# Optimization experiments

Hardware: AMD Instinct MI355X
Metric: run time of the kernel (lower is better)

Reference implementation:

```python
import jax, jax.numpy as jnp
import numpy as np
import math

B, S, D, H = 2, 2048, 2048, 16
DH = D // H
NEG = -1e9  # finite stand-in for -inf so fully-masked rows stay NaN-free


def setup_inputs() -> dict:
    key = jax.random.key(0)
    ks = jax.random.split(key, 6)
    x = jax.random.normal(ks[0], (B, S, D), dtype=jnp.float32)
    key_padding_mask = jax.random.randint(ks[1], (B, S), 0, 2, dtype=jnp.int32)
    Wqkv_w = jax.random.normal(ks[2], (3 * D, D), dtype=jnp.float32) / math.sqrt(D)
    Wqkv_b = jnp.zeros((3 * D,), dtype=jnp.float32)
    out_w = jax.random.normal(ks[3], (D, D), dtype=jnp.float32) / math.sqrt(D)
    out_b = jnp.zeros((D,), dtype=jnp.float32)
    return {"x": x, "key_padding_mask": key_padding_mask, "Wqkv_w": Wqkv_w,
            "Wqkv_b": Wqkv_b, "out_w": out_w, "out_b": out_b}


def reference(x, key_padding_mask, Wqkv_w, Wqkv_b, out_w, out_b):
    b, s, d = x.shape
    # fused QKV projection (torch Linear: y = x @ W.T + b)
    qkv = (x @ Wqkv_w.T + Wqkv_b).reshape(b, s, 3, H, DH)
    q, k, v = qkv[:, :, 0], qkv[:, :, 1], qkv[:, :, 2]  # each [b, s, H, DH]
    scale = 1.0 / math.sqrt(DH)
    scores = jnp.einsum('bqhd,bkhd->bhqk', q, k) * scale  # [b, H, s, s]
    # additive key-padding bias: -inf where mask == 0 (finite NEG for stability)
    pad_bias = jnp.where(key_padding_mask == 0, NEG, 0.0).astype(x.dtype)[:, None, None, :]
    # causal mask: key index > query index is disallowed
    causal = jnp.where(jnp.arange(s)[None, :] > jnp.arange(s)[:, None], NEG, 0.0).astype(x.dtype)
    p = jax.nn.softmax(scores + pad_bias + causal, axis=-1)
    attn = jnp.einsum('bhqk,bkhd->bqhd', p, v).reshape(b, s, d)
    return attn @ out_w.T + out_b
```

## Files before the change

kernel.cpp:

```cpp
#include <hip/hip_runtime.h>
#include <cstdint>

typedef unsigned short u16;
typedef __attribute__((ext_vector_type(8))) short short8v;
typedef __attribute__((ext_vector_type(8))) unsigned short u16x8;
typedef __attribute__((ext_vector_type(4))) float floatx4;

typedef unsigned int __attribute__((address_space(1))) as1_u32;
typedef unsigned int __attribute__((address_space(3))) as3_u32;

__device__ __forceinline__ u16 f2bf(float f) {
  union { float f; unsigned u; } v; v.f = f;
  unsigned r = v.u + 0x7FFFu + ((v.u >> 16) & 1u);
  return (u16)(r >> 16);
}

__device__ __forceinline__ unsigned cvt_pk_bf16(float lo, float hi) {
  unsigned r;
  asm("v_cvt_pk_bf16_f32 %0, %1, %2" : "=v"(r) : "v"(lo), "v"(hi));
  return r;
}

__device__ __forceinline__ void gload16(void* lds, const void* g) {
  __builtin_amdgcn_global_load_lds((as1_u32*)(uintptr_t)g, (as3_u32*)(uintptr_t)lds, 16, 0, 0);
}

__global__ __launch_bounds__(256)
void f2bf3_kernel(const float* __restrict__ in0, u16* __restrict__ out0, int n0,
                  const float* __restrict__ in1, u16* __restrict__ out1, int n1,
                  const float* __restrict__ in2, u16* __restrict__ out2, int n2) {
  int i = blockIdx.x * 256 + threadIdx.x;
  const int stride = gridDim.x * 256;
  const int total = n0 + n1 + n2;
  for (; i < total; i += stride) {
    const float* src; u16* dst; int k;
    if (i < n0)            { src = in0; dst = out0; k = i; }
    else if (i < n0 + n1)  { src = in1; dst = out1; k = i - n0; }
    else                   { src = in2; dst = out2; k = i - n0 - n1; }
    float4 v = ((const float4*)src)[k];
    ushort4 o;
    o.x = f2bf(v.x); o.y = f2bf(v.y); o.z = f2bf(v.z); o.w = f2bf(v.w);
    ((ushort4*)dst)[k] = o;
  }
}

__global__ __launch_bounds__(512, 4)
void gemm_qkv(const u16* __restrict__ A, const u16* __restrict__ B,
              const float* __restrict__ bias, u16* __restrict__ C,
              u16* __restrict__ VT, int M, int N, int K) {
  __shared__ u16 Al[3][4096];
  __shared__ u16 Bl[3][8192];
  const int tid = threadIdx.x;
  const int wid = tid >> 6, lane = tid & 63;
  const int wr = wid >> 2, wc = wid & 3;
  const int li = lane & 15, lg = lane >> 4;
  const int nwg = gridDim.x;
  const int bid = blockIdx.x;
  const int swz = (bid & 7) * (nwg >> 3) + (bid >> 3);
  const int mcnt = M >> 7;
  const int bm = swz % mcnt, bn = swz / mcnt;
  const int brow = bm * 128, bcol = bn * 256;
  const int NT = K >> 5;

  const int P = tid * 16;
  const int pr = P >> 7;
  const int innerLog = (P & 127) ^ ((pr & 7) << 4);
  const int srow = (pr << 1) + (innerLog >> 6);
  const int skb = innerLog & 63;
  const u16* aS = A + (size_t)(brow + srow) * K + (skb >> 1);
  const u16* bS = B + (size_t)(bcol + srow) * K + (skb >> 1);

#define STG(slot, kt_)                                                          \
  {                                                                             \
    const u16* a_ = aS + (kt_) * 32;                                            \
    const u16* b_ = bS + (kt_) * 32;                                            \
    gload16((char*)&Al[slot][0] + P, a_);                                       \
    gload16((char*)&Bl[slot][0] + P, b_);                                       \
    gload16((char*)&Bl[slot][0] + 8192 + P, b_ + (size_t)128 * K);              \
  }

  floatx4 acc[4][4];
#pragma unroll
  for (int m = 0; m < 4; ++m)
#pragma unroll
    for (int n = 0; n < 4; ++n) acc[m][n] = floatx4{0.f, 0.f, 0.f, 0.f};

  const int fxor = ((li >> 1) & 7) << 4;
  const int finner = (((li & 1) << 6) + (lg << 4)) ^ fxor;
  const int aoff = (wr * 32 + (li >> 1)) * 128 + finner;
  const int boff = (wc * 32 + (li >> 1)) * 128 + finner;

  STG(0, 0);
  STG(1, 1);
  asm volatile("s_waitcnt vmcnt(3)" ::: "memory");
  __builtin_amdgcn_s_barrier();

  int sl = 0;
  for (int t = 0; t < NT; ++t) {
    const char* Ab = (const char*)&Al[sl][0];
    const char* Bb = (const char*)&Bl[sl][0];
    short8v af[4], bf[4];
#pragma unroll
    for (int m = 0; m < 4; ++m) af[m] = *(const short8v*)(Ab + aoff + m * 1024);
#pragma unroll
    for (int n = 0; n < 4; ++n) bf[n] = *(const short8v*)(Bb + boff + n * 1024);

    int s2 = sl + 2; if (s2 >= 3) s2 -= 3;
    if (t + 2 < NT) STG(s2, t + 2);

    __builtin_amdgcn_s_setprio(1);
#pragma unroll
    for (int m = 0; m < 4; ++m)
#pragma unroll
      for (int n = 0; n < 4; ++n)
        acc[m][n] = __builtin_amdgcn_mfma_f32_16x16x32_bf16(af[m], bf[n], acc[m][n], 0, 0, 0);
    __builtin_amdgcn_s_setprio(0);

    if (t + 2 < NT)      asm volatile("s_waitcnt vmcnt(3)" ::: "memory");
    else if (t + 1 < NT) asm volatile("s_waitcnt vmcnt(0)" ::: "memory");
    __builtin_amdgcn_s_barrier();
    sl = (sl + 1 == 3) ? 0 : sl + 1;
  }
#undef STG

  const int crow0 = brow + wr * 64 + lg * 4;
  const int ccol0 = bcol + wc * 64 + li;
  if (bcol >= 4096) {
    const int bb = crow0 >> 11;
    const int s0b = (crow0 & 2047);
#pragma unroll
    for (int n = 0; n < 4; ++n) {
      const int vcol = ccol0 - 4096 + n * 16;
      const int hh = vcol >> 7, dh = vcol & 127;
      const float bv = bias[ccol0 + n * 16];
      u16* drow = VT + ((size_t)(bb * 16 + hh) * 128 + dh) * 2048;
#pragma unroll
      for (int m = 0; m < 4; ++m) {
        ushort4 o;
        o.x = f2bf(acc[m][n][0] + bv);
        o.y = f2bf(acc[m][n][1] + bv);
        o.z = f2bf(acc[m][n][2] + bv);
        o.w = f2bf(acc[m][n][3] + bv);
        *(ushort4*)(drow + s0b + m * 16) = o;
      }
    }
  } else {
#pragma unroll
    for (int n = 0; n < 4; ++n) {
      const float bv = bias[ccol0 + n * 16];
#pragma unroll
      for (int m = 0; m < 4; ++m) {
#pragma unroll
        for (int j = 0; j < 4; ++j) {
          const float v = acc[m][n][j] + bv;
          C[(size_t)(crow0 + m * 16 + j) * N + (ccol0 + n * 16)] = f2bf(v);
        }
      }
    }
  }
}

template <int OUT_BF16>
__global__ __launch_bounds__(256, 4)
void gemm_s(const u16* __restrict__ A, const u16* __restrict__ B,
            const float* __restrict__ bias, void* __restrict__ C,
            int M, int N, int K) {
  __shared__ u16 Al[3][4096];
  __shared__ u16 Bl[3][4096];
  const int tid = threadIdx.x;
  const int wid = tid >> 6, lane = tid & 63;
  const int wr = wid >> 1, wc = wid & 1;
  const int li = lane & 15, lg = lane >> 4;
  const int nwg = gridDim.x;
  const int bid = blockIdx.x;
  const int swz = (bid & 7) * (nwg >> 3) + (bid >> 3);
  const int mcnt = M >> 7;
  const int bm = swz % mcnt, bn = swz / mcnt;
  const int brow = bm * 128, bcol = bn * 128;
  const int NT = K >> 5;

  const int P = tid * 16;
  const int pr = P >> 7;
  const int innerLog = (P & 127) ^ ((pr & 7) << 4);
  const int srow = (pr << 1) + (innerLog >> 6);
  const int skb = innerLog & 63;
  const u16* aS = A + (size_t)(brow + srow) * K + (skb >> 1);
  const u16* bS = B + (size_t)(bcol + srow) * K + (skb >> 1);

#define STG(slot, kt_)                                                          \
  {                                                                             \
    const u16* a_ = aS + (kt_) * 32;                                            \
    const u16* b_ = bS + (kt_) * 32;                                            \
    gload16((char*)&Al[slot][0] + P, a_);                                       \
    gload16((char*)&Al[slot][0] + 4096 + P, a_ + (size_t)64 * K);               \
    gload16((char*)&Bl[slot][0] + P, b_);                                       \
    gload16((char*)&Bl[slot][0] + 4096 + P, b_ + (size_t)64 * K);               \
  }

  floatx4 acc[4][4];
#pragma unroll
  for (int m = 0; m < 4; ++m)
#pragma unroll
    for (int n = 0; n < 4; ++n) acc[m][n] = floatx4{0.f, 0.f, 0.f, 0.f};

  const int fxor = ((li >> 1) & 7) << 4;
  const int finner = (((li & 1) << 6) + (lg << 4)) ^ fxor;
  const int aoff = (wr * 32 + (li >> 1)) * 128 + finner;
  const int boff = (wc * 32 + (li >> 1)) * 128 + finner;

  STG(0, 0);
  STG(1, 1);
  asm volatile("s_waitcnt vmcnt(4)" ::: "memory");
  __builtin_amdgcn_s_barrier();

  int sl = 0;
  for (int t = 0; t < NT; ++t) {
    const char* Ab = (const char*)&Al[sl][0];
    const char* Bb = (const char*)&Bl[sl][0];
    short8v af[4], bf[4];
#pragma unroll
    for (int m = 0; m < 4; ++m) af[m] = *(const short8v*)(Ab + aoff + m * 1024);
#pragma unroll
    for (int n = 0; n < 4; ++n) bf[n] = *(const short8v*)(Bb + boff + n * 1024);

    int s2 = sl + 2; if (s2 >= 3) s2 -= 3;
    if (t + 2 < NT) STG(s2, t + 2);

    __builtin_amdgcn_s_setprio(1);
#pragma unroll
    for (int m = 0; m < 4; ++m)
#pragma unroll
      for (int n = 0; n < 4; ++n)
        acc[m][n] = __builtin_amdgcn_mfma_f32_16x16x32_bf16(af[m], bf[n], acc[m][n], 0, 0, 0);
    __builtin_amdgcn_s_setprio(0);

    if (t + 2 < NT)      asm volatile("s_waitcnt vmcnt(4)" ::: "memory");
    else if (t + 1 < NT) asm volatile("s_waitcnt vmcnt(0)" ::: "memory");
    __builtin_amdgcn_s_barrier();
    sl = (sl + 1 == 3) ? 0 : sl + 1;
  }
#undef STG

  const int crow0 = brow + wr * 64 + lg * 4;
  const int ccol0 = bcol + wc * 64 + li;
#pragma unroll
  for (int n = 0; n < 4; ++n) {
    const float bv = bias[ccol0 + n * 16];
#pragma unroll
    for (int m = 0; m < 4; ++m) {
#pragma unroll
      for (int j = 0; j < 4; ++j) {
        const float v = acc[m][n][j] + bv;
        const size_t idx = (size_t)(crow0 + m * 16 + j) * N + (ccol0 + n * 16);
        if (OUT_BF16) ((u16*)C)[idx] = f2bf(v);
        else          ((float*)C)[idx] = v;
      }
    }
  }
}

__global__ __launch_bounds__(256, 2)
void attn_fused(const u16* __restrict__ qkv, const u16* __restrict__ vt,
                const int* __restrict__ kpm, u16* __restrict__ attn_out) {
  constexpr int S = 2048, DQ = 6144;
  __shared__ u16 Kl[2][64 * 128];
  __shared__ u16 Vl[128 * 64];
  __shared__ float mskf[2048];
  __shared__ int s_any;
  const int bx = blockIdx.x, by = blockIdx.y;
  const int qt = ((by >> 4) & 1) ? bx : (15 - bx);
  const int bh = by;
  const int b = bh >> 4, h = bh & 15;
  const int tid = threadIdx.x, wave = tid >> 6, lane = tid & 63;
  const int lg = lane >> 4, li = lane & 15;
  const int qrow0 = qt * 128 + wave * 32;

  const u16* Qb = qkv + (size_t)b * S * DQ + h * 128;
  const u16* Kb = Qb + 2048;
  const u16* Vtb = vt + (size_t)bh * 128 * 2048;
  const int* mrow = kpm + b * S;

  if (tid == 0) s_any = 0;
  __syncthreads();
  {
    int a = 0;
    for (int j = tid; j < 2048; j += 256) {
      const int mv = mrow[j];
      mskf[j] = mv ? 0.f : -1.0e9f;
      if (mv && j <= qt * 128) a = 1;
    }
    if (a) s_any = 1;
  }
  __syncthreads();
  const int anyv = s_any;
  const int nt = anyv ? (2 * qt + 2) : 32;
  const int causalFromW = anyv ? (qrow0 >> 6) : 0;

  short8v qb[2][4];
#pragma unroll
  for (int m = 0; m < 2; ++m) {
    const u16* qp = Qb + (size_t)(qrow0 + m * 16 + li) * DQ + lg * 8;
#pragma unroll
    for (int kk = 0; kk < 4; ++kk) qb[m][kk] = *(const short8v*)(qp + kk * 32);
  }
  asm volatile("s_waitcnt vmcnt(0)" ::: "memory");

  float mM[2], lSum[2];
  floatx4 oa[2][8];
#pragma unroll
  for (int m = 0; m < 2; ++m) {
    mM[m] = -3.0e38f; lSum[m] = 0.f;
#pragma unroll
    for (int n = 0; n < 8; ++n) oa[m][n] = floatx4{0.f, 0.f, 0.f, 0.f};
  }

  const u16* kSrc[4]; const u16* vSrc[4];
#pragma unroll
  for (int i = 0; i < 4; ++i) {
    const int L = i * 4096 + tid * 16;
    const int r = L >> 8;
    const int c = ((L & 255) ^ ((r & 7) << 4)) >> 1;
    kSrc[i] = Kb + (size_t)r * DQ + c;
    const int d = L >> 7;
    const int sv = ((L & 127) ^ ((d & 7) << 4)) >> 1;
    vSrc[i] = Vtb + (size_t)d * 2048 + sv;
  }

#define STAGE_K(buf, kt_)                                                      \
  {                                                                            \
    const int kv0_ = (kt_) * 64;                                               \
    _Pragma("unroll")                                                          \
    for (int i = 0; i < 4; ++i)                                                \
      gload16((char*)Kl + (buf) * 16384 + i * 4096 + tid * 16,                 \
              kSrc[i] + (size_t)kv0_ * DQ);                                    \
  }
#define STAGE_V(kt_)                                                           \
  {                                                                            \
    const int kv0_ = (kt_) * 64;                                               \
    _Pragma("unroll")                                                          \
    for (int i = 0; i < 4; ++i)                                                \
      gload16((char*)Vl + i * 4096 + tid * 16, vSrc[i] + kv0_);                \
  }

  const float scale = 0.08838834764831845f;

  STAGE_K(0, 0);
  STAGE_V(0);

  for (int kt = 0; kt < nt; ++kt) {
    const int cur = kt & 1;
    const int kv0 = kt * 64;
    if (kt + 1 < nt) {
      STAGE_K(cur ^ 1, kt + 1);
      asm volatile("s_waitcnt vmcnt(8)" ::: "memory");
    } else {
      asm volatile("s_waitcnt vmcnt(4)" ::: "memory");
    }
    __builtin_amdgcn_s_barrier();

    const char* Kcur = (const char*)Kl + cur * 16384;

    floatx4 sc[2][4];
#pragma unroll
    for (int n = 0; n < 4; ++n) { sc[0][n] = floatx4{0,0,0,0}; sc[1][n] = floatx4{0,0,0,0}; }
    __builtin_amdgcn_s_setprio(1);
#pragma unroll
    for (int n = 0; n < 4; ++n) {
      const int r = n * 16 + li;
#pragma unroll
      for (int kk = 0; kk < 4; ++kk) {
        const int byteo = (r * 256 + kk * 64 + lg * 16) ^ ((r & 7) << 4);
        const short8v kf = *(const short8v*)(Kcur + byteo);
        sc[0][n] = __builtin_amdgcn_mfma_f32_16x16x32_bf16(kf, qb[0][kk], sc[0][n], 0, 0, 0);
        sc[1][n] = __builtin_amdgcn_mfma_f32_16x16x32_bf16(kf, qb[1][kk], sc[1][n], 0, 0, 0);
      }
    }
    __builtin_amdgcn_s_setprio(0);

    floatx4 pbv[4];
#pragma unroll
    for (int n = 0; n < 4; ++n)
      pbv[n] = *(const floatx4*)&mskf[kv0 + n * 16 + lg * 4];
    const bool cz = (kt >= causalFromW);

    short8v pf[2][2];
#pragma unroll
    for (int m = 0; m < 2; ++m) {
      const int q_l = qrow0 + m * 16 + li;
      float tmax = -3.0e38f;
#pragma unroll
      for (int n = 0; n < 4; ++n)
#pragma unroll
        for (int j = 0; j < 4; ++j) {
          float s = sc[m][n][j] * scale + pbv[n][j];
          if (cz && (kv0 + n * 16 + lg * 4 + j > q_l)) s -= 1.0e9f;
          sc[m][n][j] = s;
          tmax = fmaxf(tmax, s);
        }
      tmax = fmaxf(tmax, __shfl_xor(tmax, 16));
      tmax = fmaxf(tmax, __shfl_xor(tmax, 32));
      const float mnew = fmaxf(mM[m], tmax);
      const float f = __expf(mM[m] - mnew);
      mM[m] = mnew;
      float rs = 0.f;
#pragma unroll
      for (int n = 0; n < 4; ++n)
#pragma unroll
        for (int j = 0; j < 4; ++j) {
          const float e = __expf(sc[m][n][j] - mnew);
          sc[m][n][j] = e; rs += e;
        }
      rs += __shfl_xor(rs, 16);
      rs += __shfl_xor(rs, 32);
      lSum[m] = lSum[m] * f + rs;
#pragma unroll
      for (int n2 = 0; n2 < 8; ++n2) oa[m][n2] *= f;

      unsigned w32[4][2];
#pragma unroll
      for (int n = 0; n < 4; ++n) {
        w32[n][0] = cvt_pk_bf16(sc[m][n][0], sc[m][n][1]);
        w32[n][1] = cvt_pk_bf16(sc[m][n][2], sc[m][n][3]);
      }
      union PF { short8v s; unsigned w[4]; } pfu[2];
#pragma unroll
      for (int kk2 = 0; kk2 < 2; ++kk2) {
#pragma unroll
        for (int hh = 0; hh < 2; ++hh) {
          unsigned u = w32[2 * kk2][hh], v = w32[2 * kk2 + 1][hh];
          asm volatile("v_permlane32_swap_b32 %0, %1" : "+v"(u), "+v"(v));
          asm volatile("v_permlane16_swap_b32 %0, %1" : "+v"(u), "+v"(v));
          pfu[kk2].w[hh] = u;
          pfu[kk2].w[2 + hh] = v;
        }
      }
      pf[m][0] = pfu[0].s;
      pf[m][1] = pfu[1].s;
    }

    if (kt + 1 < nt) asm volatile("s_waitcnt vmcnt(4)" ::: "memory");
    else             asm volatile("s_waitcnt vmcnt(0)" ::: "memory");
    __builtin_amdgcn_s_barrier();

    __builtin_amdgcn_s_setprio(1);
#pragma unroll
    for (int kk2 = 0; kk2 < 2; ++kk2) {
#pragma unroll
      for (int n2 = 0; n2 < 8; ++n2) {
        const int d = n2 * 16 + li;
        const int vbyte = (d * 128 + kk2 * 64 + lg * 16) ^ ((d & 7) << 4);
        const short8v vf = *(const short8v*)((const char*)Vl + vbyte);
        oa[0][n2] = __builtin_amdgcn_mfma_f32_16x16x32_bf16(vf, pf[0][kk2], oa[0][n2], 0, 0, 0);
        oa[1][n2] = __builtin_amdgcn_mfma_f32_16x16x32_bf16(vf, pf[1][kk2], oa[1][n2], 0, 0, 0);
      }
    }
    __builtin_amdgcn_s_setprio(0);
    __builtin_amdgcn_s_barrier();
    if (kt + 1 < nt) STAGE_V(kt + 1);
  }

  {
    char* Ol = (char*)Kl + wave * 8192;
#pragma unroll
    for (int m = 0; m < 2; ++m) {
      const float inv = 1.0f / lSum[m];
      const int q_ = m * 16 + li;
#pragma unroll
      for (int n2 = 0; n2 < 8; ++n2) {
        unsigned lo = cvt_pk_bf16(oa[m][n2][0] * inv, oa[m][n2][1] * inv);
        unsigned hi = cvt_pk_bf16(oa[m][n2][2] * inv, oa[m][n2][3] * inv);
        const int byteo = (q_ * 256 + n2 * 32 + lg * 8) ^ ((q_ & 7) << 4);
        uint2 pr2; pr2.x = lo; pr2.y = hi;
        *(uint2*)(Ol + byteo) = pr2;
      }
    }
    asm volatile("s_waitcnt lgkmcnt(0)" ::: "memory");
#pragma unroll
    for (int rr = 0; rr < 4; ++rr) {
      const int r = rr * 8 + (lane >> 3);
      const size_t grow = (size_t)(b * 2048 + qt * 128 + wave * 32 + r) * 2048 + h * 128;
#pragma unroll
      for (int s2 = 0; s2 < 2; ++s2) {
        const int byteo = (r * 256 + (lane & 7) * 32 + s2 * 16) ^ ((r & 7) << 4);
        const u16x8 val = *(const u16x8*)(Ol + byteo);
        *(u16x8*)&attn_out[grow + (lane & 7) * 16 + s2 * 8] = val;
      }
    }
  }
#undef STAGE_K
#undef STAGE_V
}

extern "C" void kernel_launch(void* const* d_in, const int* in_sizes, int n_in,
                              void* d_out, int out_size, void* d_ws, size_t ws_size,
                              hipStream_t stream) {
  const float* x    = (const float*)d_in[0];
  const int*   kpm  = (const int*)d_in[1];
  const float* wqkv = (const float*)d_in[2];
  const float* bqkv = (const float*)d_in[3];
  const float* wout = (const float*)d_in[4];
  const float* bout = (const float*)d_in[5];
  float* out = (float*)d_out;

  char* ws = (char*)d_ws;
  u16* xbf   = (u16*)(ws);
  u16* wqbf  = (u16*)(ws + (16u << 20));
  u16* wobf  = (u16*)(ws + (40u << 20));
  u16* qkvb  = (u16*)(ws + (48u << 20));
  u16* vtb   = (u16*)(ws + (96u << 20));
  u16* attnb = (u16*)(ws + (112u << 20));

  f2bf3_kernel<<<2048, 256, 0, stream>>>(x,    xbf,  4096 * 2048 / 4,
                                         wqkv, wqbf, 6144 * 2048 / 4,
                                         wout, wobf, 2048 * 2048 / 4);

  gemm_qkv<<<768, 512, 0, stream>>>(xbf, wqbf, bqkv, qkvb, vtb, 4096, 6144, 2048);
  attn_fused<<<dim3(16, 32), 256, 0, stream>>>(qkvb, vtb, kpm, attnb);
  gemm_s<0><<<512, 256, 0, stream>>>(attnb, wobf, bout, out, 4096, 2048, 2048);
}
```

Measured before the change: 279.7 us.

## Double-buffer V tiles with K prefetch and use raw exp2 softmax

Adds a second V buffer in LDS so the next tile's K and V both load during the current iteration. This removes the mid-iteration wait and barrier before the PV matmul. It also folds log2(e) into the scale and mask constants so softmax can use the raw v_exp_f32 instruction instead of __expf. The cost is more LDS per block, which may reduce occupancy, and a full vmcnt(0) wait on the last tile.

```diff
diff --git a/kernel.cpp b/kernel.cpp
--- a/kernel.cpp
+++ b/kernel.cpp
@@ -18,6 +18,12 @@
 __device__ __forceinline__ unsigned cvt_pk_bf16(float lo, float hi) {
   unsigned r;
   asm("v_cvt_pk_bf16_f32 %0, %1, %2" : "=v"(r) : "v"(lo), "v"(hi));
+  return r;
+}
+
+__device__ __forceinline__ float exp2_raw(float x) {
+  float r;
+  asm("v_exp_f32 %0, %1" : "=v"(r) : "v"(x));
   return r;
 }
 
@@ -264,7 +270,7 @@
                 const int* __restrict__ kpm, u16* __restrict__ attn_out) {
   constexpr int S = 2048, DQ = 6144;
   __shared__ u16 Kl[2][64 * 128];
-  __shared__ u16 Vl[128 * 64];
+  __shared__ u16 Vl[2][64 * 128];
   __shared__ float mskf[2048];
   __shared__ int s_any;
   const int bx = blockIdx.x, by = blockIdx.y;
@@ -286,7 +292,7 @@
     int a = 0;
     for (int j = tid; j < 2048; j += 256) {
       const int mv = mrow[j];
-      mskf[j] = mv ? 0.f : -1.0e9f;
+      mskf[j] = mv ? 0.f : -1.4426950e9f;
       if (mv && j <= qt * 128) a = 1;
     }
     if (a) s_any = 1;
@@ -326,39 +332,36 @@
     vSrc[i] = Vtb + (size_t)d * 2048 + sv;
   }
 
-#define STAGE_K(buf, kt_)                                                      \
+#define STAGE_KV(buf, kt_)                                                     \
   {                                                                            \
     const int kv0_ = (kt_) * 64;                                               \
     _Pragma("unroll")                                                          \
     for (int i = 0; i < 4; ++i)                                                \
       gload16((char*)Kl + (buf) * 16384 + i * 4096 + tid * 16,                 \
               kSrc[i] + (size_t)kv0_ * DQ);                                    \
-  }
-#define STAGE_V(kt_)                                                           \
-  {                                                                            \
-    const int kv0_ = (kt_) * 64;                                               \
     _Pragma("unroll")                                                          \
     for (int i = 0; i < 4; ++i)                                                \
-      gload16((char*)Vl + i * 4096 + tid * 16, vSrc[i] + kv0_);                \
-  }
-
-  const float scale = 0.08838834764831845f;
-
-  STAGE_K(0, 0);
-  STAGE_V(0);
+      gload16((char*)Vl + (buf) * 16384 + i * 4096 + tid * 16,                 \
+              vSrc[i] + kv0_);                                                 \
+  }
+
+  const float scale2 = 0.12751743f;
+
+  STAGE_KV(0, 0);
 
   for (int kt = 0; kt < nt; ++kt) {
     const int cur = kt & 1;
     const int kv0 = kt * 64;
     if (kt + 1 < nt) {
-      STAGE_K(cur ^ 1, kt + 1);
+      STAGE_KV(cur ^ 1, kt + 1);
       asm volatile("s_waitcnt vmcnt(8)" ::: "memory");
     } else {
-      asm volatile("s_waitcnt vmcnt(4)" ::: "memory");
+      asm volatile("s_waitcnt vmcnt(0)" ::: "memory");
     }
     __builtin_amdgcn_s_barrier();
 
     const char* Kcur = (const char*)Kl + cur * 16384;
+    const char* Vcur = (const char*)Vl + cur * 16384;
 
     floatx4 sc[2][4];
 #pragma unroll
@@ -392,22 +395,22 @@
       for (int n = 0; n < 4; ++n)
 #pragma unroll
         for (int j = 0; j < 4; ++j) {
-          float s = sc[m][n][j] * scale + pbv[n][j];
-          if (cz && (kv0 + n * 16 + lg * 4 + j > q_l)) s -= 1.0e9f;
+          float s = sc[m][n][j] * scale2 + pbv[n][j];
+          if (cz && (kv0 + n * 16 + lg * 4 + j > q_l)) s -= 1.4426950e9f;
           sc[m][n][j] = s;
           tmax = fmaxf(tmax, s);
         }
       tmax = fmaxf(tmax, __shfl_xor(tmax, 16));
       tmax = fmaxf(tmax, __shfl_xor(tmax, 32));
       const float mnew = fmaxf(mM[m], tmax);
-      const float f = __expf(mM[m] - mnew);
+      const float f = exp2_raw(mM[m] - mnew);
       mM[m] = mnew;
       float rs = 0.f;
 #pragma unroll
       for (int n = 0; n < 4; ++n)
 #pragma unroll
         for (int j = 0; j < 4; ++j) {
-          const float e = __expf(sc[m][n][j] - mnew);
+          const float e = exp2_raw(sc[m][n][j] - mnew);
           sc[m][n][j] = e; rs += e;
         }
       rs += __shfl_xor(rs, 16);
@@ -438,10 +441,6 @@
       pf[m][1] = pfu[1].s;
     }
 
-    if (kt + 1 < nt) asm volatile("s_waitcnt vmcnt(4)" ::: "memory");
-    else             asm volatile("s_waitcnt vmcnt(0)" ::: "memory");
-    __builtin_amdgcn_s_barrier();
-
     __builtin_amdgcn_s_setprio(1);
 #pragma unroll
     for (int kk2 = 0; kk2 < 2; ++kk2) {
@@ -449,14 +448,13 @@
       for (int n2 = 0; n2 < 8; ++n2) {
         const int d = n2 * 16 + li;
         const int vbyte = (d * 128 + kk2 * 64 + lg * 16) ^ ((d & 7) << 4);
-        const short8v vf = *(const short8v*)((const char*)Vl + vbyte);
+        const short8v vf = *(const short8v*)(Vcur + vbyte);
         oa[0][n2] = __builtin_amdgcn_mfma_f32_16x16x32_bf16(vf, pf[0][kk2], oa[0][n2], 0, 0, 0);
         oa[1][n2] = __builtin_amdgcn_mfma_f32_16x16x32_bf16(vf, pf[1][kk2], oa[1][n2], 0, 0, 0);
       }
     }
     __builtin_amdgcn_s_setprio(0);
     __builtin_amdgcn_s_barrier();
-    if (kt + 1 < nt) STAGE_V(kt + 1);
   }
 
   {
@@ -487,8 +485,7 @@
       }
     }
   }
-#undef STAGE_K
-#undef STAGE_V
+#undef STAGE_KV
 }
 
 extern "C" void kernel_launch(void* const* d_in, const int* in_sizes, int n_in,
```

Measured after the change: 276.9 us, median of 2. No clear change (-1.0%).
